# Performance work log

Measured on AMD Instinct MI355X. Metric: run time of the kernel, lower is better.

Reference implementation:

```python
import jax, jax.numpy as jnp
import numpy as np

DEPTH = 4  # truncation depth of the signature


def setup_inputs() -> dict:
    key = jax.random.key(0)
    # (N, L, C) batch of paths
    path = jax.random.normal(key, (64, 512, 8), dtype=jnp.float32)
    return {"path": path}


def _signature(path, depth):
    """Truncated path signature: exp(dx_1) (x) exp(dx_2) (x) ... via Chen's relation.

    Signature state is kept as a tuple of flattened tensor levels, level k has
    shape (N, C**k). Combining a signature S with exp(z) gives, at level k:
        sum_{j=0}^{k} S_{k-j} (x) z^{(x)j} / j!   (with S_0 = 1)
    """
    N, L, C = path.shape
    # increments, scanned over the stream dim: (L-1, N, C)
    diffs = jnp.swapaxes(path[:, 1:] - path[:, :-1], 0, 1)

    def step(sig, z):
        # powers[j-1] = z^{(x)j} / j!, flattened to (N, C**j)
        powers = [z]
        for j in range(2, depth + 1):
            powers.append((powers[-1][:, :, None] * z[:, None, :]).reshape(N, -1) / j)
        new = []
        for k in range(1, depth + 1):
            term = sig[k - 1] + powers[k - 1]  # j=0 and j=k terms
            for j in range(1, k):
                # S_{k-j} (x) z^{(x)j}/j!
                term = term + (sig[k - j - 1][:, :, None]
                               * powers[j - 1][:, None, :]).reshape(N, C ** k)
            new.append(term)
        return tuple(new), None

    # identity element of the tensor algebra: all levels >= 1 are zero
    init = tuple(jnp.zeros((N, C ** k), dtype=path.dtype) for k in range(1, depth + 1))
    sig, _ = jax.lax.scan(step, init, diffs)
    # (N, C + C^2 + ... + C^depth)
    return jnp.concatenate(sig, axis=-1)


def reference(path) -> jnp.ndarray:
    return _signature(path, DEPTH)
```

## Files before the change

### kernel.cpp

```cpp
#include <hip/hip_runtime.h>


typedef float f2 __attribute__((ext_vector_type(2)));

#define NB 64
#define LP 512
#define SIG 4680
#define O2 8
#define O3 72
#define O4 584
#define SB 648

#define A3IDX(pq, r) (72 + (pq) * 9 + (r))
#define B3IDX(x, y, z) (72 + (x) * 72 + (y) * 8 + (z))

__device__ __forceinline__ f2 mkf2(float x, float y) { f2 r; r[0] = x; r[1] = y; return r; }

__global__ __launch_bounds__(256) void k1_sig(const float* __restrict__ path,
                                              float* __restrict__ ws)
{
    __shared__ __align__(16) float zbuf[128 * 8];
    __shared__ __align__(16) float sA0[SB], sB1[SB], sA2[SB], sB3[SB];
    __shared__ __align__(16) float sPA[SB], sPB[SB];
    __shared__ __align__(16) float4 sT[4][1024];

    const int tid = threadIdx.x;
    const int n = blockIdx.x >> 2;
    const int g = blockIdx.x & 3;

    {
        const int r = tid >> 1, hh = tid & 1;
        const int t = g * 128 + r;
        const float4* p4 = (const float4*)path + (size_t)n * (LP * 2);
        float4 z4 = make_float4(0.f, 0.f, 0.f, 0.f);
        if (t < LP - 1) {
            float4 x0 = p4[t * 2 + hh];
            float4 x1 = p4[t * 2 + 2 + hh];
            z4 = make_float4(x1.x - x0.x, x1.y - x0.y, x1.z - x0.z, x1.w - x0.w);
        }
        ((float4*)zbuf)[tid] = z4;
    }
    __syncthreads();

    const int w = tid >> 6, l = tid & 63;
    const int a = l >> 3, b = l & 7;
    const int f0 = 2 * tid;

    float s1 = 0.f, s2 = 0.f;
    f2 s3p[4], s4p[32];
    #pragma unroll
    for (int i = 0; i < 4; ++i) s3p[i] = mkf2(0.f, 0.f);
    #pragma unroll
    for (int e = 0; e < 32; ++e) s4p[e] = mkf2(0.f, 0.f);

    const float* zw = zbuf + w * (32 * 8);
    #pragma unroll 4
    for (int s = 0; s < 32; ++s) {
        const float* zs = zw + s * 8;
        f2 zp[4];
        #pragma unroll
        for (int j = 0; j < 4; ++j) zp[j] = ((const f2*)zs)[j];
        const float za  = zs[a];
        const float zbv = zs[b];
        const float B4 = zbv * (za * (1.f/24.f) + s1 * (1.f/6.f)) + s2 * 0.5f;
        const float G3 = zbv * (za * (1.f/6.f)  + s1 * 0.5f)      + s2;
        f2 Acp[4];
        #pragma unroll
        for (int i = 0; i < 4; ++i) Acp[i] = B4 * zp[i] + s3p[i];
        #pragma unroll
        for (int c = 0; c < 8; ++c) {
            const float Ac = Acp[c >> 1][c & 1];
            #pragma unroll
            for (int j = 0; j < 4; ++j) s4p[c * 4 + j] += Ac * zp[j];
        }
        #pragma unroll
        for (int i = 0; i < 4; ++i) s3p[i] += G3 * zp[i];
        s2 += zbv * (za * 0.5f + s1);
        s1 += za;
    }

    if ((w & 1) == 0) {
        float* SA = (w == 0) ? sA0 : sA2;
        if (b == 0) SA[a] = s1;
        SA[O2 + l] = s2;
        #pragma unroll
        for (int c = 0; c < 8; ++c) SA[A3IDX(l, c)] = s3p[c >> 1][c & 1];
    } else {
        float* SL = (w == 1) ? sB1 : sB3;
        if (b == 0) SL[a] = s1;
        SL[O2 + l] = s2;
        *(float4*)&SL[B3IDX(a, b, 0)] = make_float4(s3p[0][0], s3p[0][1], s3p[1][0], s3p[1][1]);
        *(float4*)&SL[B3IDX(a, b, 4)] = make_float4(s3p[2][0], s3p[2][1], s3p[3][0], s3p[3][1]);
    }
    #pragma unroll
    for (int i = 0; i < 16; ++i)
        sT[w][i * 64 + l] = make_float4(s4p[2*i][0], s4p[2*i][1], s4p[2*i+1][0], s4p[2*i+1][1]);
    __syncthreads();

    {
        const int h  = tid >> 7;
        const int ht = tid & 127;
        const int hi = ht >> 6;
        const int la = (ht >> 3) & 7, lb = ht & 7;
        const float* SA  = h ? sA2 : sA0;
        const float* SBb = h ? sB3 : sB1;
        float4* TA = sT[h ? 2 : 0];
        const float4* TB = sT[h ? 3 : 1];
        const int dh = hi * 4;
        const float A1  = SA[la];
        const float A2v = SA[O2 + la * 8 + lb];
        f2 b1p[2];
        *(float4*)&b1p[0] = *(const float4*)(SBb + dh);
        #pragma unroll
        for (int k = 0; k < 8; ++k) {
            const int f = k * 128 + ht;
            const float A3c = SA[A3IDX(la * 8 + lb, k)];
            f2 b2p[2], b3p[2];
            *(float4*)&b2p[0] = *(const float4*)(SBb + O2 + k * 8 + dh);
            *(float4*)&b3p[0] = *(const float4*)(SBb + B3IDX(lb, k, dh));
            float4 av = TA[f], bv = TB[f];
            f2 r0 = mkf2(av.x, av.y) + mkf2(bv.x, bv.y)
                  + A3c * b1p[0] + A2v * b2p[0] + A1 * b3p[0];
            f2 r1 = mkf2(av.z, av.w) + mkf2(bv.z, bv.w)
                  + A3c * b1p[1] + A2v * b2p[1] + A1 * b3p[1];
            TA[f] = make_float4(r0[0], r0[1], r1[0], r1[1]);
        }
        float* OP = h ? sPB : sPA;
        const int f3 = ht * 4;
        const int pp = f3 >> 6, qq = (f3 >> 3) & 7, rr = f3 & 7;
        const float A1p  = SA[pp];
        const float A2pq = SA[O2 + pp * 8 + qq];
        f2 bb1[2], bb2[2], bb3[2];
        *(float4*)&bb1[0] = *(const float4*)(SBb + rr);
        *(float4*)&bb2[0] = *(const float4*)(SBb + O2 + qq * 8 + rr);
        *(float4*)&bb3[0] = *(const float4*)(SBb + B3IDX(pp, qq, rr));
        float o[4];
        #pragma unroll
        for (int j = 0; j < 4; ++j)
            o[j] = SA[A3IDX(pp * 8 + qq, rr + j)] + bb3[j >> 1][j & 1]
                 + A2pq * bb1[j >> 1][j & 1] + A1p * bb2[j >> 1][j & 1];
        if (h == 0) {
            #pragma unroll
            for (int j = 0; j < 4; ++j) OP[A3IDX(pp * 8 + qq, rr + j)] = o[j];
        } else {
            *(float4*)&OP[B3IDX(pp, qq, rr)] = make_float4(o[0], o[1], o[2], o[3]);
        }
        if (ht < 64) OP[O2 + ht] = SA[O2 + ht] + SBb[O2 + ht] + SA[ht >> 3] * SBb[ht & 7];
        if (ht < 8)  OP[ht] = SA[ht] + SBb[ht];
    }
    __syncthreads();

    {
        const int c0 = 2 * w;
        f2 a4[8], b4[8];
        #pragma unroll
        for (int k = 0; k < 4; ++k) {
            float4 v = sT[0][(w * 4 + k) * 64 + l];
            a4[2*k] = mkf2(v.x, v.y); a4[2*k+1] = mkf2(v.z, v.w);
            float4 u = sT[2][(w * 4 + k) * 64 + l];
            b4[2*k] = mkf2(u.x, u.y); b4[2*k+1] = mkf2(u.z, u.w);
        }
        const float A1  = sPA[a];
        const float A2v = sPA[O2 + a * 8 + b];
        const float A3_0 = sPA[A3IDX(a * 8 + b, c0)];
        const float A3_1 = sPA[A3IDX(a * 8 + b, c0 + 1)];
        f2 b1p[4], b2p[8], b3p[8];
        *(float4*)&b1p[0] = *(const float4*)(sPB);
        *(float4*)&b1p[2] = *(const float4*)(sPB + 4);
        #pragma unroll
        for (int i = 0; i < 4; ++i) {
            *(float4*)&b2p[2*i] = *(const float4*)(sPB + O2 + c0 * 8 + 4 * i);
            *(float4*)&b3p[2*i] = *(const float4*)(sPB + B3IDX(b, c0, 0) + 4 * i);
        }
        #pragma unroll
        for (int cc = 0; cc < 2; ++cc) {
            const float A3c = cc ? A3_1 : A3_0;
            #pragma unroll
            for (int j = 0; j < 4; ++j)
                a4[cc*4+j] += b4[cc*4+j] + A3c * b1p[j]
                            + A2v * b2p[cc*4+j] + A1 * b3p[cc*4+j];
        }

        float* dst = ws + (size_t)blockIdx.x * SIG;
        float4* dT = (float4*)(dst + O4);
        #pragma unroll
        for (int k = 0; k < 4; ++k)
            dT[(w * 4 + k) * 64 + l] =
                make_float4(a4[2*k][0], a4[2*k][1], a4[2*k+1][0], a4[2*k+1][1]);
        const int pp = f0 >> 6, qq = (f0 >> 3) & 7, rr = f0 & 7;
        const float A1p  = sPA[pp];
        const float A2pq = sPA[O2 + pp * 8 + qq];
        dst[O3 + f0]     = sPA[A3IDX(pp*8+qq, rr)]     + sPB[B3IDX(pp, qq, rr)]
                         + A2pq * sPB[rr]     + A1p * sPB[O2 + qq * 8 + rr];
        dst[O3 + f0 + 1] = sPA[A3IDX(pp*8+qq, rr + 1)] + sPB[B3IDX(pp, qq, rr + 1)]
                         + A2pq * sPB[rr + 1] + A1p * sPB[O2 + qq * 8 + rr + 1];
        if (tid < 64) dst[O2 + tid] = sPA[O2 + tid] + sPB[O2 + tid] + sPA[tid >> 3] * sPB[tid & 7];
        if (tid < 8)  dst[tid] = sPA[tid] + sPB[tid];
    }
}

__global__ __launch_bounds__(256) void k2_final(const float* __restrict__ ws,
                                                float* __restrict__ out)
{
    __shared__ __align__(16) float sA0[SB], sB1[SB], sA2[SB], sB3[SB];
    __shared__ __align__(16) float sPA[SB], sPB[SB];

    const int tid = threadIdx.x;
    const int n  = blockIdx.x >> 2;
    const int w4 = blockIdx.x & 3;
    const int a = tid >> 5, b = (tid >> 2) & 7, q = tid & 3;
    const int cc = q >> 1, dh4 = q & 1;
    const int c  = 2 * w4 + cc;
    const int dh = dh4 * 4;
    const int f0 = 2 * tid;
    const float* base = ws + (size_t)n * 4 * SIG;
    const float* s0 = base;
    const float* s1g = base + SIG;
    const float* s2g = base + 2 * SIG;
    const float* s3g = base + 3 * SIG;

    const int ti = (w4 * 4 + cc * 2 + dh4) * 64 + (a * 8 + b);
    f2 r0[2], r1[2], r2[2], r3[2];
    {
        float4 u0 = ((const float4*)(s0 + O4))[ti];
        r0[0] = mkf2(u0.x, u0.y); r0[1] = mkf2(u0.z, u0.w);
        float4 u1 = ((const float4*)(s1g + O4))[ti];
        r1[0] = mkf2(u1.x, u1.y); r1[1] = mkf2(u1.z, u1.w);
        float4 u2 = ((const float4*)(s2g + O4))[ti];
        r2[0] = mkf2(u2.x, u2.y); r2[1] = mkf2(u2.z, u2.w);
        float4 u3 = ((const float4*)(s3g + O4))[ti];
        r3[0] = mkf2(u3.x, u3.y); r3[1] = mkf2(u3.z, u3.w);
    }

    if (tid < O3) { sA0[tid] = s0[tid]; sA2[tid] = s2g[tid]; }
    sA0[A3IDX(f0 >> 3, f0 & 7)]       = s0[O3 + f0];
    sA0[A3IDX(f0 >> 3, (f0 & 7) + 1)] = s0[O3 + f0 + 1];
    sA2[A3IDX(f0 >> 3, f0 & 7)]       = s2g[O3 + f0];
    sA2[A3IDX(f0 >> 3, (f0 & 7) + 1)] = s2g[O3 + f0 + 1];
    if (tid < 146) {
        int d4 = (tid < 18) ? tid : 18 + ((tid - 18) >> 4) * 18 + ((tid - 18) & 15);
        ((float4*)sB1)[d4] = ((const float4*)s1g)[tid];
        ((float4*)sB3)[d4] = ((const float4*)s3g)[tid];
    }
    __syncthreads();

    f2 p01[2], p23[2];
    {
        const float A1a = sA0[a], A2a = sA0[O2 + a * 8 + b];
        const float A3a = sA0[A3IDX(a * 8 + b, c)];
        f2 b1p[2], b2p[2], b3p[2];
        *(float4*)&b1p[0] = *(const float4*)(sB1 + dh);
        *(float4*)&b2p[0] = *(const float4*)(sB1 + O2 + c * 8 + dh);
        *(float4*)&b3p[0] = *(const float4*)(sB1 + B3IDX(b, c, dh));
        #pragma unroll
        for (int j = 0; j < 2; ++j)
            p01[j] = r0[j] + r1[j] + A3a * b1p[j] + A2a * b2p[j] + A1a * b3p[j];
        const float A1b = sA2[a], A2b = sA2[O2 + a * 8 + b];
        const float A3b = sA2[A3IDX(a * 8 + b, c)];
        f2 c1p[2], c2p[2], c3p[2];
        *(float4*)&c1p[0] = *(const float4*)(sB3 + dh);
        *(float4*)&c2p[0] = *(const float4*)(sB3 + O2 + c * 8 + dh);
        *(float4*)&c3p[0] = *(const float4*)(sB3 + B3IDX(b, c, dh));
        #pragma unroll
        for (int j = 0; j < 2; ++j)
            p23[j] = r2[j] + r3[j] + A3b * c1p[j] + A2b * c2p[j] + A1b * c3p[j];

        const int h  = tid >> 7;
        const int ht = tid & 127;
        const float* SA  = h ? sA2 : sA0;
        const float* SBb = h ? sB3 : sB1;
        float* OP = h ? sPB : sPA;
        const int f3 = ht * 4;
        const int pp = f3 >> 6, qq = (f3 >> 3) & 7, rr = f3 & 7;
        const float A1p  = SA[pp];
        const float A2pq = SA[O2 + pp * 8 + qq];
        f2 bb1[2], bb2[2], bb3[2];
        *(float4*)&bb1[0] = *(const float4*)(SBb + rr);
        *(float4*)&bb2[0] = *(const float4*)(SBb + O2 + qq * 8 + rr);
        *(float4*)&bb3[0] = *(const float4*)(SBb + B3IDX(pp, qq, rr));
        float o[4];
        #pragma unroll
        for (int j = 0; j < 4; ++j)
            o[j] = SA[A3IDX(pp * 8 + qq, rr + j)] + bb3[j >> 1][j & 1]
                 + A2pq * bb1[j >> 1][j & 1] + A1p * bb2[j >> 1][j & 1];
        if (h == 0) {
            #pragma unroll
            for (int j = 0; j < 4; ++j) OP[A3IDX(pp * 8 + qq, rr + j)] = o[j];
        } else {
            *(float4*)&OP[B3IDX(pp, qq, rr)] = make_float4(o[0], o[1], o[2], o[3]);
        }
        if (ht < 64) OP[O2 + ht] = SA[O2 + ht] + SBb[O2 + ht] + SA[ht >> 3] * SBb[ht & 7];
        if (ht < 8)  OP[ht] = SA[ht] + SBb[ht];
    }
    __syncthreads();

    float* dst = out + (size_t)n * SIG;
    {
        const float A1  = sPA[a];
        const float A2v = sPA[O2 + a * 8 + b];
        const float A3c = sPA[A3IDX(a * 8 + b, c)];
        f2 b1p[2], b2p[2], b3p[2];
        *(float4*)&b1p[0] = *(const float4*)(sPB + dh);
        *(float4*)&b2p[0] = *(const float4*)(sPB + O2 + c * 8 + dh);
        *(float4*)&b3p[0] = *(const float4*)(sPB + B3IDX(b, c, dh));
        f2 rf[2];
        #pragma unroll
        for (int j = 0; j < 2; ++j)
            rf[j] = p01[j] + p23[j] + A3c * b1p[j] + A2v * b2p[j] + A1 * b3p[j];
        ((float4*)(dst + O4))[((a * 8 + b) * 8 + c) * 2 + dh4] =
            make_float4(rf[0][0], rf[0][1], rf[1][0], rf[1][1]);
    }
    if (w4 == 0) {
        const int pp = f0 >> 6, qq = (f0 >> 3) & 7, rr = f0 & 7;
        const float A1p  = sPA[pp];
        const float A2pq = sPA[O2 + pp * 8 + qq];
        dst[O3 + f0]     = sPA[A3IDX(pp*8+qq, rr)]     + sPB[B3IDX(pp, qq, rr)]
                         + A2pq * sPB[rr]     + A1p * sPB[O2 + qq * 8 + rr];
        dst[O3 + f0 + 1] = sPA[A3IDX(pp*8+qq, rr + 1)] + sPB[B3IDX(pp, qq, rr + 1)]
                         + A2pq * sPB[rr + 1] + A1p * sPB[O2 + qq * 8 + rr + 1];
        if (tid < 64) dst[O2 + tid] = sPA[O2 + tid] + sPB[O2 + tid] + sPA[tid >> 3] * sPB[tid & 7];
        if (tid < 8)  dst[tid] = sPA[tid] + sPB[tid];
    }
}

extern "C" void kernel_launch(void* const* d_in, const int* in_sizes, int n_in,
                              void* d_out, int out_size, void* d_ws, size_t ws_size,
                              hipStream_t stream) {
    const float* path = (const float*)d_in[0];
    float* out = (float*)d_out;
    float* ws  = (float*)d_ws;

    k1_sig<<<NB * 4, 256, 0, stream>>>(path, ws);
    k2_final<<<NB * 4, 256, 0, stream>>>(ws, out);
}
```

Baseline: 18.33 us.

## Split each path into eight time chunks and combine with a tree reduction

The first kernel now launches eight blocks per path, each scanning sixteen steps per wave instead of thirty-two, so the serial sequential-scan work per block halves and more blocks are available to fill the GPU. The combine kernel reads eight partial signatures and merges them with a three-level Chen-product tree held in shared memory. The first kernel aliases its increment buffer with the product scratch to save shared memory. The cost is twice the workspace traffic, more shared memory in the combine kernel, and extra combine arithmetic and barriers.

```diff
diff --git a/kernel.cpp b/kernel.cpp
--- a/kernel.cpp
+++ b/kernel.cpp
@@ -19,18 +19,20 @@
 __global__ __launch_bounds__(256) void k1_sig(const float* __restrict__ path,
                                               float* __restrict__ ws)
 {
-    __shared__ __align__(16) float zbuf[128 * 8];
+    __shared__ __align__(16) float uZP[2 * SB];
     __shared__ __align__(16) float sA0[SB], sB1[SB], sA2[SB], sB3[SB];
-    __shared__ __align__(16) float sPA[SB], sPB[SB];
     __shared__ __align__(16) float4 sT[4][1024];
+    float* const zbuf = uZP;
+    float* const sPA  = uZP;
+    float* const sPB  = uZP + SB;
 
     const int tid = threadIdx.x;
-    const int n = blockIdx.x >> 2;
-    const int g = blockIdx.x & 3;
-
-    {
+    const int n = blockIdx.x >> 3;
+    const int g = blockIdx.x & 7;
+
+    if (tid < 128) {
         const int r = tid >> 1, hh = tid & 1;
-        const int t = g * 128 + r;
+        const int t = g * 64 + r;
         const float4* p4 = (const float4*)path + (size_t)n * (LP * 2);
         float4 z4 = make_float4(0.f, 0.f, 0.f, 0.f);
         if (t < LP - 1) {
@@ -53,9 +55,9 @@
     #pragma unroll
     for (int e = 0; e < 32; ++e) s4p[e] = mkf2(0.f, 0.f);
 
-    const float* zw = zbuf + w * (32 * 8);
+    const float* zw = zbuf + w * (16 * 8);
     #pragma unroll 4
-    for (int s = 0; s < 32; ++s) {
+    for (int s = 0; s < 16; ++s) {
         const float* zs = zw + s * 8;
         f2 zp[4];
         #pragma unroll
@@ -199,11 +201,46 @@
     }
 }
 
+__device__ __forceinline__ void l4slice(const float* PA, const float* PB,
+                                        const f2 x[2], const f2 y[2], f2 r[2],
+                                        int a, int b, int c, int dh)
+{
+    const float A1  = PA[a];
+    const float A2v = PA[O2 + a * 8 + b];
+    const float A3c = PA[A3IDX(a * 8 + b, c)];
+    f2 b1p[2], b2p[2], b3p[2];
+    *(float4*)&b1p[0] = *(const float4*)(PB + dh);
+    *(float4*)&b2p[0] = *(const float4*)(PB + O2 + c * 8 + dh);
+    *(float4*)&b3p[0] = *(const float4*)(PB + B3IDX(b, c, dh));
+    #pragma unroll
+    for (int j = 0; j < 2; ++j)
+        r[j] = x[j] + y[j] + A3c * b1p[j] + A2v * b2p[j] + A1 * b3p[j];
+}
+
+template<bool ALAY>
+__device__ __forceinline__ void l123prod(const float* PA, const float* PB,
+                                         float* OUT, int tid)
+{
+    const int f0 = 2 * tid;
+    const int pp = f0 >> 6, qq = (f0 >> 3) & 7, rr = f0 & 7;
+    const float A1p  = PA[pp];
+    const float A2pq = PA[O2 + pp * 8 + qq];
+    #pragma unroll
+    for (int j = 0; j < 2; ++j) {
+        const float v = PA[A3IDX(pp * 8 + qq, rr + j)] + PB[B3IDX(pp, qq, rr + j)]
+                      + A2pq * PB[rr + j] + A1p * PB[O2 + qq * 8 + rr + j];
+        if (ALAY) OUT[A3IDX(pp * 8 + qq, rr + j)] = v;
+        else      OUT[B3IDX(pp, qq, rr + j)] = v;
+    }
+    if (tid < 64) OUT[O2 + tid] = PA[O2 + tid] + PB[O2 + tid] + PA[tid >> 3] * PB[tid & 7];
+    if (tid < 8)  OUT[tid] = PA[tid] + PB[tid];
+}
+
 __global__ __launch_bounds__(256) void k2_final(const float* __restrict__ ws,
                                                 float* __restrict__ out)
 {
-    __shared__ __align__(16) float sA0[SB], sB1[SB], sA2[SB], sB3[SB];
-    __shared__ __align__(16) float sPA[SB], sPB[SB];
+    __shared__ __align__(16) float sAe[4][SB], sBo[4][SB];
+    __shared__ __align__(16) float sP[4][SB];
 
     const int tid = threadIdx.x;
     const int n  = blockIdx.x >> 2;
@@ -213,113 +250,67 @@
     const int c  = 2 * w4 + cc;
     const int dh = dh4 * 4;
     const int f0 = 2 * tid;
-    const float* base = ws + (size_t)n * 4 * SIG;
-    const float* s0 = base;
-    const float* s1g = base + SIG;
-    const float* s2g = base + 2 * SIG;
-    const float* s3g = base + 3 * SIG;
+    const float* base = ws + (size_t)n * 8 * SIG;
 
     const int ti = (w4 * 4 + cc * 2 + dh4) * 64 + (a * 8 + b);
-    f2 r0[2], r1[2], r2[2], r3[2];
-    {
-        float4 u0 = ((const float4*)(s0 + O4))[ti];
-        r0[0] = mkf2(u0.x, u0.y); r0[1] = mkf2(u0.z, u0.w);
-        float4 u1 = ((const float4*)(s1g + O4))[ti];
-        r1[0] = mkf2(u1.x, u1.y); r1[1] = mkf2(u1.z, u1.w);
-        float4 u2 = ((const float4*)(s2g + O4))[ti];
-        r2[0] = mkf2(u2.x, u2.y); r2[1] = mkf2(u2.z, u2.w);
-        float4 u3 = ((const float4*)(s3g + O4))[ti];
-        r3[0] = mkf2(u3.x, u3.y); r3[1] = mkf2(u3.z, u3.w);
-    }
-
-    if (tid < O3) { sA0[tid] = s0[tid]; sA2[tid] = s2g[tid]; }
-    sA0[A3IDX(f0 >> 3, f0 & 7)]       = s0[O3 + f0];
-    sA0[A3IDX(f0 >> 3, (f0 & 7) + 1)] = s0[O3 + f0 + 1];
-    sA2[A3IDX(f0 >> 3, f0 & 7)]       = s2g[O3 + f0];
-    sA2[A3IDX(f0 >> 3, (f0 & 7) + 1)] = s2g[O3 + f0 + 1];
-    if (tid < 146) {
-        int d4 = (tid < 18) ? tid : 18 + ((tid - 18) >> 4) * 18 + ((tid - 18) & 15);
-        ((float4*)sB1)[d4] = ((const float4*)s1g)[tid];
-        ((float4*)sB3)[d4] = ((const float4*)s3g)[tid];
-    }
-    __syncthreads();
-
-    f2 p01[2], p23[2];
-    {
-        const float A1a = sA0[a], A2a = sA0[O2 + a * 8 + b];
-        const float A3a = sA0[A3IDX(a * 8 + b, c)];
-        f2 b1p[2], b2p[2], b3p[2];
-        *(float4*)&b1p[0] = *(const float4*)(sB1 + dh);
-        *(float4*)&b2p[0] = *(const float4*)(sB1 + O2 + c * 8 + dh);
-        *(float4*)&b3p[0] = *(const float4*)(sB1 + B3IDX(b, c, dh));
-        #pragma unroll
-        for (int j = 0; j < 2; ++j)
-            p01[j] = r0[j] + r1[j] + A3a * b1p[j] + A2a * b2p[j] + A1a * b3p[j];
-        const float A1b = sA2[a], A2b = sA2[O2 + a * 8 + b];
-        const float A3b = sA2[A3IDX(a * 8 + b, c)];
-        f2 c1p[2], c2p[2], c3p[2];
-        *(float4*)&c1p[0] = *(const float4*)(sB3 + dh);
-        *(float4*)&c2p[0] = *(const float4*)(sB3 + O2 + c * 8 + dh);
-        *(float4*)&c3p[0] = *(const float4*)(sB3 + B3IDX(b, c, dh));
-        #pragma unroll
-        for (int j = 0; j < 2; ++j)
-            p23[j] = r2[j] + r3[j] + A3b * c1p[j] + A2b * c2p[j] + A1b * c3p[j];
-
-        const int h  = tid >> 7;
-        const int ht = tid & 127;
-        const float* SA  = h ? sA2 : sA0;
-        const float* SBb = h ? sB3 : sB1;
-        float* OP = h ? sPB : sPA;
-        const int f3 = ht * 4;
-        const int pp = f3 >> 6, qq = (f3 >> 3) & 7, rr = f3 & 7;
-        const float A1p  = SA[pp];
-        const float A2pq = SA[O2 + pp * 8 + qq];
-        f2 bb1[2], bb2[2], bb3[2];
-        *(float4*)&bb1[0] = *(const float4*)(SBb + rr);
-        *(float4*)&bb2[0] = *(const float4*)(SBb + O2 + qq * 8 + rr);
-        *(float4*)&bb3[0] = *(const float4*)(SBb + B3IDX(pp, qq, rr));
-        float o[4];
-        #pragma unroll
-        for (int j = 0; j < 4; ++j)
-            o[j] = SA[A3IDX(pp * 8 + qq, rr + j)] + bb3[j >> 1][j & 1]
-                 + A2pq * bb1[j >> 1][j & 1] + A1p * bb2[j >> 1][j & 1];
-        if (h == 0) {
-            #pragma unroll
-            for (int j = 0; j < 4; ++j) OP[A3IDX(pp * 8 + qq, rr + j)] = o[j];
-        } else {
-            *(float4*)&OP[B3IDX(pp, qq, rr)] = make_float4(o[0], o[1], o[2], o[3]);
-        }
-        if (ht < 64) OP[O2 + ht] = SA[O2 + ht] + SBb[O2 + ht] + SA[ht >> 3] * SBb[ht & 7];
-        if (ht < 8)  OP[ht] = SA[ht] + SBb[ht];
-    }
+    f2 r[8][2];
+    #pragma unroll
+    for (int m = 0; m < 8; ++m) {
+        float4 u = ((const float4*)(base + (size_t)m * SIG + O4))[ti];
+        r[m][0] = mkf2(u.x, u.y); r[m][1] = mkf2(u.z, u.w);
+    }
+
+    #pragma unroll
+    for (int i = 0; i < 4; ++i) {
+        const float* se = base + (size_t)(2 * i) * SIG;
+        const float* so = base + (size_t)(2 * i + 1) * SIG;
+        if (tid < O3) sAe[i][tid] = se[tid];
+        sAe[i][A3IDX(f0 >> 3, f0 & 7)]       = se[O3 + f0];
+        sAe[i][A3IDX(f0 >> 3, (f0 & 7) + 1)] = se[O3 + f0 + 1];
+        if (tid < 146) {
+            int d4 = (tid < 18) ? tid : 18 + ((tid - 18) >> 4) * 18 + ((tid - 18) & 15);
+            ((float4*)sBo[i])[d4] = ((const float4*)so)[tid];
+        }
+    }
+    __syncthreads();
+
+    f2 p01[2], p23[2], p45[2], p67[2];
+    l4slice(sAe[0], sBo[0], r[0], r[1], p01, a, b, c, dh);
+    l4slice(sAe[1], sBo[1], r[2], r[3], p23, a, b, c, dh);
+    l4slice(sAe[2], sBo[2], r[4], r[5], p45, a, b, c, dh);
+    l4slice(sAe[3], sBo[3], r[6], r[7], p67, a, b, c, dh);
+    l123prod<true >(sAe[0], sBo[0], sP[0], tid);
+    l123prod<false>(sAe[1], sBo[1], sP[1], tid);
+    l123prod<true >(sAe[2], sBo[2], sP[2], tid);
+    l123prod<false>(sAe[3], sBo[3], sP[3], tid);
+    __syncthreads();
+
+    f2 pAB[2], pCD[2];
+    l4slice(sP[0], sP[1], p01, p23, pAB, a, b, c, dh);
+    l4slice(sP[2], sP[3], p45, p67, pCD, a, b, c, dh);
+    l123prod<true >(sP[0], sP[1], sAe[0], tid);
+    l123prod<false>(sP[2], sP[3], sBo[0], tid);
     __syncthreads();
 
     float* dst = out + (size_t)n * SIG;
     {
-        const float A1  = sPA[a];
-        const float A2v = sPA[O2 + a * 8 + b];
-        const float A3c = sPA[A3IDX(a * 8 + b, c)];
-        f2 b1p[2], b2p[2], b3p[2];
-        *(float4*)&b1p[0] = *(const float4*)(sPB + dh);
-        *(float4*)&b2p[0] = *(const float4*)(sPB + O2 + c * 8 + dh);
-        *(float4*)&b3p[0] = *(const float4*)(sPB + B3IDX(b, c, dh));
         f2 rf[2];
-        #pragma unroll
-        for (int j = 0; j < 2; ++j)
-            rf[j] = p01[j] + p23[j] + A3c * b1p[j] + A2v * b2p[j] + A1 * b3p[j];
+        l4slice(sAe[0], sBo[0], pAB, pCD, rf, a, b, c, dh);
         ((float4*)(dst + O4))[((a * 8 + b) * 8 + c) * 2 + dh4] =
             make_float4(rf[0][0], rf[0][1], rf[1][0], rf[1][1]);
     }
     if (w4 == 0) {
         const int pp = f0 >> 6, qq = (f0 >> 3) & 7, rr = f0 & 7;
-        const float A1p  = sPA[pp];
-        const float A2pq = sPA[O2 + pp * 8 + qq];
-        dst[O3 + f0]     = sPA[A3IDX(pp*8+qq, rr)]     + sPB[B3IDX(pp, qq, rr)]
-                         + A2pq * sPB[rr]     + A1p * sPB[O2 + qq * 8 + rr];
-        dst[O3 + f0 + 1] = sPA[A3IDX(pp*8+qq, rr + 1)] + sPB[B3IDX(pp, qq, rr + 1)]
-                         + A2pq * sPB[rr + 1] + A1p * sPB[O2 + qq * 8 + rr + 1];
-        if (tid < 64) dst[O2 + tid] = sPA[O2 + tid] + sPB[O2 + tid] + sPA[tid >> 3] * sPB[tid & 7];
-        if (tid < 8)  dst[tid] = sPA[tid] + sPB[tid];
+        const float* PA = sAe[0];
+        const float* PB = sBo[0];
+        const float A1p  = PA[pp];
+        const float A2pq = PA[O2 + pp * 8 + qq];
+        dst[O3 + f0]     = PA[A3IDX(pp*8+qq, rr)]     + PB[B3IDX(pp, qq, rr)]
+                         + A2pq * PB[rr]     + A1p * PB[O2 + qq * 8 + rr];
+        dst[O3 + f0 + 1] = PA[A3IDX(pp*8+qq, rr + 1)] + PB[B3IDX(pp, qq, rr + 1)]
+                         + A2pq * PB[rr + 1] + A1p * PB[O2 + qq * 8 + rr + 1];
+        if (tid < 64) dst[O2 + tid] = PA[O2 + tid] + PB[O2 + tid] + PA[tid >> 3] * PB[tid & 7];
+        if (tid < 8)  dst[tid] = PA[tid] + PB[tid];
     }
 }
 
@@ -330,6 +321,6 @@
     float* out = (float*)d_out;
     float* ws  = (float*)d_ws;
 
-    k1_sig<<<NB * 4, 256, 0, stream>>>(path, ws);
+    k1_sig<<<NB * 8, 256, 0, stream>>>(path, ws);
     k2_final<<<NB * 4, 256, 0, stream>>>(ws, out);
 }
```

Result: slower. 23.89 us (+30.3%).
